# Performance work log

Hardware: AMD Instinct MI355X
Metric: run time of the kernel (lower is better)

Reference implementation:

```python
import jax, jax.numpy as jnp
import numpy as np

SEQ_LEN = 32
B, H, E, HID = 2048, 512, 512, 16
BN_EPS = 1e-5

def _mlp(x, w1, b1, g, bt, m, v, w2, b2):
    # Linear -> BatchNorm1d(eval) -> ReLU -> Linear
    h = x @ w1 + b1
    h = (h - m) * jax.lax.rsqrt(v + BN_EPS) * g + bt
    h = jnp.maximum(h, 0.0)
    return h @ w2 + b2

def setup_inputs() -> dict:
    key = jax.random.key(0)
    ks = jax.random.split(key, 24)
    def rn(k, shp, s=0.05):
        return jax.random.normal(k, shp, dtype=jnp.float32) * s
    inp = {
        'last_pos': jax.random.uniform(ks[0], (B, 2), dtype=jnp.float32),
        'hh': rn(ks[1], (1, B, H), 1.0),
        'ch': rn(ks[2], (1, B, H), 1.0),
        'se_w1': rn(ks[3], (2, HID)),
        'se_b1': rn(ks[4], (HID,)),
        'se_g': jax.random.uniform(ks[5], (HID,), dtype=jnp.float32) + 0.5,
        'se_bt': rn(ks[6], (HID,)),
        'se_m': rn(ks[7], (HID,)),
        'se_v': jax.random.uniform(ks[8], (HID,), dtype=jnp.float32) + 0.5,
        'se_w2': rn(ks[9], (HID, E)),
        'se_b2': rn(ks[10], (E,)),
        'w_ih': rn(ks[11], (4 * H, E)),
        'w_hh': rn(ks[12], (4 * H, H)),
        'b_ih': rn(ks[13], (4 * H,)),
        'b_hh': rn(ks[14], (4 * H,)),
        'hp_w1': rn(ks[15], (H, HID)),
        'hp_b1': rn(ks[16], (HID,)),
        'hp_g': jax.random.uniform(ks[17], (HID,), dtype=jnp.float32) + 0.5,
        'hp_bt': rn(ks[18], (HID,)),
        'hp_m': rn(ks[19], (HID,)),
        'hp_v': jax.random.uniform(ks[20], (HID,), dtype=jnp.float32) + 0.5,
        'hp_w2': rn(ks[21], (HID, 2)),
        'hp_b2': rn(ks[22], (2,)),
    }
    return inp

def reference(last_pos, hh, ch, se_w1, se_b1, se_g, se_bt, se_m, se_v, se_w2, se_b2,
              w_ih, w_hh, b_ih, b_hh,
              hp_w1, hp_b1, hp_g, hp_bt, hp_m, hp_v, hp_w2, hp_b2):
    h0, c0 = hh[0], ch[0]  # num_layers == 1

    def step(carry, _):
        h, c, lp = carry
        x = _mlp(lp, se_w1, se_b1, se_g, se_bt, se_m, se_v, se_w2, se_b2)  # [B,E]
        gates = x @ w_ih.T + b_ih + h @ w_hh.T + b_hh                      # [B,4H]
        i, f, g, o = jnp.split(gates, 4, axis=-1)
        i = jax.nn.sigmoid(i)
        f = jax.nn.sigmoid(f)
        g = jnp.tanh(g)
        o = jax.nn.sigmoid(o)
        c = f * c + i * g
        h = o * jnp.tanh(c)
        pos_rel = _mlp(h, hp_w1, hp_b1, hp_g, hp_bt, hp_m, hp_v, hp_w2, hp_b2)  # [B,2]
        # relative_to_abs on a length-1 sequence == pos_rel + last_pos, then sigmoid
        lp = jax.nn.sigmoid(pos_rel + lp)
        return (h, c, lp), lp

    _, traj = jax.lax.scan(step, (h0, c0, last_pos), None, length=SEQ_LEN)
    return traj  # [seq_len, batch, 2]
```

## Files before the change

### kernel.cpp

```cpp
#include <hip/hip_runtime.h>


#define TSEQ  32
#define BATCH 2048
#define HDIM  512
#define NBLK  256
#define NTHR  512
#define DEPTH 8

typedef __bf16 bf16x8 __attribute__((ext_vector_type(8)));
typedef float  f32x16 __attribute__((ext_vector_type(16)));
typedef unsigned u32x4 __attribute__((ext_vector_type(4)));
typedef unsigned long long u64;

#define BS_OFF     0
#define HPW_OFF    131072
#define UNI_OFF    147456
#define H1_OFF     157696
#define LPS_OFF    161792
#define PRM_OFF    162816
#define LDS_TOTAL  163360
#define W1T_OFF    32768
#define BT_OFF     41472

#define WS_FLAGS  0
#define WS_HATOM  2048

__device__ __forceinline__ unsigned f2bf(float f) {
  unsigned u = __float_as_uint(f);
  u += 0x7fffu + ((u >> 16) & 1u);
  return u >> 16;
}
__device__ __forceinline__ void st8(void* p, u64 v) {
  __hip_atomic_store((u64*)p, v, __ATOMIC_RELAXED, __HIP_MEMORY_SCOPE_AGENT);
}
__device__ __forceinline__ unsigned ld4(const unsigned* p) {
  return __hip_atomic_load(p, __ATOMIC_RELAXED, __HIP_MEMORY_SCOPE_AGENT);
}
__device__ __forceinline__ void st4(unsigned* p, unsigned v) {
  __hip_atomic_store(p, v, __ATOMIC_RELAXED, __HIP_MEMORY_SCOPE_AGENT);
}
__device__ __forceinline__ u32x4 ld16_dev(const void* p) {
  u32x4 r;
  asm volatile("global_load_dwordx4 %0, %1, off sc0 sc1"
               : "=&v"(r) : "v"(p) : "memory");
  return r;
}
__device__ __forceinline__ void vm_drain() {
  asm volatile("s_waitcnt vmcnt(0)" ::: "memory");
}
#define WAITV(n) do { asm volatile("s_waitcnt vmcnt(" #n ")" ::: "memory"); \
                      __builtin_amdgcn_sched_barrier(0); } while (0)

#define QB(x, imm) __uint_as_float((unsigned)__builtin_amdgcn_mov_dpp((int)__float_as_uint(x), imm, 0xF, 0xF, true))

struct KParams {
  const float *last_pos, *hh, *ch0, *w_hh, *w_ih, *b_ih, *b_hh;
  const float *se_w1, *se_b1, *se_g, *se_bt, *se_m, *se_v, *se_w2, *se_b2;
  const float *hp_w1, *hp_b1, *hp_g, *hp_bt, *hp_m, *hp_v, *hp_w2, *hp_b2;
  char* hatom;
  unsigned* flags;
  float* out;
};

__global__ __launch_bounds__(NTHR, 2) void decoder_persist(KParams p) {
  extern __shared__ char lds[];
  const int tid  = threadIdx.x;
  const int lane = tid & 63;
  const int wid  = tid >> 6;
  const int wm   = wid >> 1;
  const int wn   = wid & 1;
  const int mt   = blockIdx.x >> 4;
  const int nt   = blockIdx.x & 15;
  const int m0   = mt * 128;

  float* prm = (float*)(lds + PRM_OFF);
  float* lps = (float*)(lds + LPS_OFF);
  float* h2s = (float*)(lds + UNI_OFF);
  unsigned short* hPsh = (unsigned short*)(lds + UNI_OFF);
  float* W1T = (float*)(lds + W1T_OFF);
  float* bT  = (float*)(lds + BT_OFF);

  const int n0 = wn * 64 + (lane & 31);
  const int n1 = n0 + 32;
  const int gate = lane & 3;
  const int khalf = lane >> 5;
  const int pj = ((tid >> 8) << 1) | ((tid >> 5) & 1);
  const int pm = ((tid >> 6) & 3) * 32 + (tid & 31);

  if (tid < 16) {
    int q = tid;
    float sA = p.se_g[q] * rsqrtf(p.se_v[q] + 1e-5f);
    prm[q]      = sA;
    prm[16 + q] = (p.se_b1[q] - p.se_m[q]) * sA + p.se_bt[q];
    float hA = p.hp_g[q] * rsqrtf(p.hp_v[q] + 1e-5f);
    prm[32 + q] = hA;
    prm[48 + q] = (p.hp_b1[q] - p.hp_m[q]) * hA + p.hp_bt[q];
  }
  if (tid < 32) { prm[64 + tid] = p.se_w1[tid]; prm[96 + tid] = p.hp_w2[tid]; }
  if (tid < 2)  { prm[128 + tid] = p.hp_b2[tid]; }
  if (tid < 256) lps[tid] = p.last_pos[(size_t)m0 * 2 + tid];

  for (int a = tid; a < 2048; a += NTHR) {
    int n = a >> 6, k8 = a & 63;
    uint4 v = {0, 0, 0, 0};
    if (n <= 16) {
      const float* src = (n < 16) ? (p.se_w2 + (size_t)n * 512 + k8 * 8)
                                  : (p.se_b2 + k8 * 8);
      v.x = f2bf(src[0]) | (f2bf(src[1]) << 16);
      v.y = f2bf(src[2]) | (f2bf(src[3]) << 16);
      v.z = f2bf(src[4]) | (f2bf(src[5]) << 16);
      v.w = f2bf(src[6]) | (f2bf(src[7]) << 16);
    }
    *(uint4*)(lds + BS_OFF + ((size_t)(n * 64 + (k8 ^ (n & 7)))) * 16) = v;
  }
  __syncthreads();

  if ((wid & 1) == 0) {
    int rloc = wm * 32 + (lane & 31);
    int grow = (rloc & 3) * 512 + nt * 32 + (rloc >> 2);
    const float* arow = p.w_ih + (size_t)grow * 512;
    f32x16 accW;
    #pragma unroll
    for (int i = 0; i < 16; ++i) accW[i] = 0.f;
    float4 pa[4], pb[4];
    #pragma unroll
    for (int j = 0; j < 4; ++j) {
      int kal = j * 2 + khalf;
      pa[j] = ((const float4*)(arow + kal * 8))[0];
      pb[j] = ((const float4*)(arow + kal * 8))[1];
    }
    #pragma unroll
    for (int c = 0; c < 32; ++c) {
      int kal = c * 2 + khalf;
      union { unsigned short s[8]; bf16x8 v; } av;
      float4 a = pa[c & 3], b = pb[c & 3];
      av.s[0] = f2bf(a.x); av.s[1] = f2bf(a.y); av.s[2] = f2bf(a.z); av.s[3] = f2bf(a.w);
      av.s[4] = f2bf(b.x); av.s[5] = f2bf(b.y); av.s[6] = f2bf(b.z); av.s[7] = f2bf(b.w);
      if (c + 4 < 32) {
        int kn = (c + 4) * 2 + khalf;
        pa[c & 3] = ((const float4*)(arow + kn * 8))[0];
        pb[c & 3] = ((const float4*)(arow + kn * 8))[1];
      }
      int q = lane & 31;
      bf16x8 bp = *(const bf16x8*)(lds + BS_OFF + (((q << 6) + (kal ^ (q & 7))) << 4));
      accW = __builtin_amdgcn_mfma_f32_32x32x16_bf16(av.v, bp, accW, 0, 0, 0);
    }
    int q = lane & 31;
    #pragma unroll
    for (int r = 0; r < 16; ++r) {
      int row = (r & 3) + 8 * (r >> 2) + 4 * khalf + wm * 32;
      if (q < 16) {
        W1T[row * 17 + q] = accW[r];
      } else if (q == 16) {
        int g2 = (row & 3) * 512 + nt * 32 + (row >> 2);
        bT[row] = accW[r] + p.b_ih[g2] + p.b_hh[g2];
      }
    }
  }
  __syncthreads();

  union BW { unsigned short s[8]; bf16x8 v; } w0f, w1f;
  #pragma unroll
  for (int j = 0; j < 8; ++j) {
    w0f.s[j] = (unsigned short)f2bf(W1T[n0 * 17 + khalf * 8 + j]);
    w1f.s[j] = (unsigned short)f2bf(W1T[n1 * 17 + khalf * 8 + j]);
  }
  float biasr[2];
  biasr[0] = bT[wn * 64 + (lane & 31)];
  biasr[1] = bT[wn * 64 + 32 + (lane & 31)];
  {
    const float* src = p.hh + (size_t)(m0 + pm) * 512 + nt * 32 + pj * 8;
    float4 f0 = ((const float4*)src)[0];
    float4 f1 = ((const float4*)src)[1];
    u64 lo = (u64)f2bf(f0.x) | ((u64)f2bf(f0.y) << 16)
           | ((u64)f2bf(f0.z) << 32) | ((u64)f2bf(f0.w) << 48);
    u64 hi = (u64)f2bf(f1.x) | ((u64)f2bf(f1.y) << 16)
           | ((u64)f2bf(f1.z) << 32) | ((u64)f2bf(f1.w) << 48);
    u64* hdst = (u64*)(p.hatom + 2097152 + mt * 131072);
    st8(hdst + (512 * nt + tid) * 2,     lo);
    st8(hdst + (512 * nt + tid) * 2 + 1, hi);
  }
  __syncthreads();
  if (tid == 0) st4(p.flags + mt * 32 + nt, 1u);

  for (int a = tid; a < 8192; a += NTHR) {
    int n = a >> 6, ka = a & 63;
    int grow = (n & 3) * 512 + nt * 32 + (n >> 2);
    const float* src = p.w_hh + (size_t)grow * 512 + ka * 8;
    uint4 v;
    v.x = f2bf(src[0]) | (f2bf(src[1]) << 16);
    v.y = f2bf(src[2]) | (f2bf(src[3]) << 16);
    v.z = f2bf(src[4]) | (f2bf(src[5]) << 16);
    v.w = f2bf(src[6]) | (f2bf(src[7]) << 16);
    *(uint4*)(lds + BS_OFF + ((size_t)(n * 64 + (ka ^ (n & 7)))) * 16) = v;
  }
  for (int a = tid; a < 1024; a += NTHR) {
    int n = a >> 6, k8 = a & 63;
    const float* src = p.hp_w1 + (size_t)(k8 * 8) * 16 + n;
    uint4 v;
    v.x = f2bf(src[0])  | (f2bf(src[16]) << 16);
    v.y = f2bf(src[32]) | (f2bf(src[48]) << 16);
    v.z = f2bf(src[64]) | (f2bf(src[80]) << 16);
    v.w = f2bf(src[96]) | (f2bf(src[112]) << 16);
    *(uint4*)(lds + HPW_OFF + ((size_t)(n * 64 + (k8 ^ (n & 7)))) * 16) = v;
  }
  float c_st[2][16];
  #pragma unroll
  for (int t2 = 0; t2 < 2; ++t2)
    #pragma unroll
    for (int r = 0; r < 16; ++r) c_st[t2][r] = 0.f;
  if ((lane & 3) == 0) {
    #pragma unroll
    for (int t2 = 0; t2 < 2; ++t2) {
      int jj = (wn * 64 + t2 * 32 + (lane & 31)) >> 2;
      #pragma unroll
      for (int r = 0; r < 16; ++r) {
        int row = (r & 3) + 8 * (r >> 2) + 4 * khalf + wm * 32;
        c_st[t2][r] = p.ch0[(size_t)(m0 + row) * 512 + nt * 32 + jj];
      }
    }
  }
  __syncthreads();

  float sA2q = 0.f, bA2q = 0.f;
  if ((lane & 31) < 16) { sA2q = prm[32 + (lane & 31)]; bA2q = prm[48 + (lane & 31)]; }
  const unsigned* fl = p.flags + mt * 32 + (lane & 15);

  for (int t = 0; t < TSEQ; ++t) {
    if (wid == 0) {
      while (!__all((int)(ld4(fl) >= (unsigned)(t + 1))))
        __builtin_amdgcn_s_sleep(2);
    }
    __syncthreads();

    f32x16 acc0, acc1, accP;
    #pragma unroll
    for (int i = 0; i < 16; ++i) { acc0[i] = 0.f; acc1[i] = 0.f; accP[i] = 0.f; }
    {
      const char* abase = p.hatom + (size_t)((t + 1) & 1) * 2097152 + mt * 131072
                          + (wm * 64 + lane) * 16;
      vm_drain();
      u32x4 pre[DEPTH];
      #pragma unroll
      for (int c = 0; c < DEPTH; ++c) pre[c] = ld16_dev(abase + c * 4096);
      union AB { u32x4 u; bf16x8 v; };
      #pragma unroll
      for (int c = 0; c < 32; ++c) {
        switch (c) {
          default: WAITV(7); break;
          case 25: WAITV(6); break;
          case 26: WAITV(5); break;
          case 27: WAITV(4); break;
          case 28: WAITV(3); break;
          case 29: WAITV(2); break;
          case 30: WAITV(1); break;
          case 31: WAITV(0); break;
        }
        AB u;
        u.u = pre[c & (DEPTH - 1)];
        if (c + DEPTH < 32)
          pre[c & (DEPTH - 1)] = ld16_dev(abase + (c + DEPTH) * 4096);
        int kal = c * 2 + khalf;
        bf16x8 b0 = *(const bf16x8*)(lds + BS_OFF + (((n0 << 6) + (kal ^ (n0 & 7))) << 4));
        bf16x8 b1 = *(const bf16x8*)(lds + BS_OFF + (((n1 << 6) + (kal ^ (n1 & 7))) << 4));
        acc0 = __builtin_amdgcn_mfma_f32_32x32x16_bf16(u.v, b0, acc0, 0, 0, 0);
        acc1 = __builtin_amdgcn_mfma_f32_32x32x16_bf16(u.v, b1, acc1, 0, 0, 0);
        if (wn == 0) {
          bf16x8 bp = {};
          if ((lane & 31) < 16)
            bp = *(const bf16x8*)(lds + HPW_OFF
                  + ((((lane & 31) << 6) + (kal ^ (lane & 7))) << 4));
          accP = __builtin_amdgcn_mfma_f32_32x32x16_bf16(u.v, bp, accP, 0, 0, 0);
        }
      }
    }

    if (t > 0) {
      if (wn == 0 && (lane & 31) < 16) {
        int q = lane & 31;
        #pragma unroll
        for (int r = 0; r < 16; ++r) {
          int row = (r & 3) + 8 * (r >> 2) + 4 * khalf + wm * 32;
          h2s[row * 20 + q] = fmaxf(accP[r] * sA2q + bA2q, 0.f);
        }
      }
      __syncthreads();
    }

    if (tid < 256) {
      int m = tid >> 1, c = tid & 1;
      float lp0, lp1;
      if (t > 0) {
        float a2 = prm[128 + c];
        const float4* hrow = (const float4*)(lds + UNI_OFF + m * 80);
        #pragma unroll
        for (int g4 = 0; g4 < 4; ++g4) {
          float4 v = hrow[g4];
          a2 += v.x * prm[96 + (g4 * 4 + 0) * 2 + c];
          a2 += v.y * prm[96 + (g4 * 4 + 1) * 2 + c];
          a2 += v.z * prm[96 + (g4 * 4 + 2) * 2 + c];
          a2 += v.w * prm[96 + (g4 * 4 + 3) * 2 + c];
        }
        float lpv = 1.f / (1.f + __expf(-(a2 + lps[tid])));
        lps[tid] = lpv;
        if (nt == 0)
          p.out[((size_t)(t - 1) * BATCH + m0 + m) * 2 + c] = lpv;
        float other = QB(lpv, 0xB1);
        lp0 = c ? other : lpv;
        lp1 = c ? lpv : other;
      } else {
        lp0 = lps[m * 2];
        lp1 = lps[m * 2 + 1];
      }
      u64 hq[2];
      #pragma unroll
      for (int half = 0; half < 2; ++half) {
        u64 w = 0;
        #pragma unroll
        for (int i = 0; i < 4; ++i) {
          int q = c * 8 + half * 4 + i;
          float z = lp0 * prm[64 + q] + lp1 * prm[80 + q];
          w |= (u64)f2bf(fmaxf(z * prm[q] + prm[16 + q], 0.f)) << (16 * i);
        }
        hq[half] = w;
      }
      u64* hd = (u64*)(lds + H1_OFF + m * 32 + c * 16);
      hd[0] = hq[0];
      hd[1] = hq[1];
    }
    __syncthreads();

    {
      bf16x8 a1 = *(const bf16x8*)(lds + H1_OFF + (wm * 32 + (lane & 31)) * 32 + khalf * 16);
      acc0 = __builtin_amdgcn_mfma_f32_32x32x16_bf16(a1, w0f.v, acc0, 0, 0, 0);
      acc1 = __builtin_amdgcn_mfma_f32_32x32x16_bf16(a1, w1f.v, acc1, 0, 0, 0);
    }

    #pragma unroll
    for (int t2 = 0; t2 < 2; ++t2) {
      float bias = biasr[t2];
      int jj = (wn * 64 + t2 * 32 + (lane & 31)) >> 2;
      float act[16];
      const f32x16& A = (t2 == 0) ? acc0 : acc1;
      #pragma unroll
      for (int r = 0; r < 16; ++r) {
        float v = A[r] + bias;
        float vv = (gate == 2) ? 2.f * v : v;
        float sg = 1.f / (1.f + __expf(-vv));
        act[r] = (gate == 2) ? 2.f * sg - 1.f : sg;
      }
      #pragma unroll
      for (int r = 0; r < 16; ++r) {
        float iv = QB(act[r], 0x00);
        float fv = QB(act[r], 0x55);
        float gv = QB(act[r], 0xAA);
        float ov = QB(act[r], 0xFF);
        float cn = fv * c_st[t2][r] + iv * gv;
        c_st[t2][r] = cn;
        float th = 2.f / (1.f + __expf(-2.f * cn)) - 1.f;
        float hn = ov * th;
        if ((lane & 3) == 0) {
          int row = (r & 3) + 8 * (r >> 2) + 4 * khalf + wm * 32;
          hPsh[row * 36 + jj] = (unsigned short)f2bf(hn);
        }
      }
    }
    __syncthreads();

    {
      const u64* hp8 = (const u64*)(lds + UNI_OFF + pm * 72 + pj * 16);
      u64* hdst = (u64*)(p.hatom + (size_t)(t & 1) * 2097152 + mt * 131072);
      st8(hdst + (512 * nt + tid) * 2,     hp8[0]);
      st8(hdst + (512 * nt + tid) * 2 + 1, hp8[1]);
    }
    __syncthreads();
    if (tid == 0) st4(p.flags + mt * 32 + nt, (unsigned)(t + 2));
  }

  {
    if (wid == 0) {
      while (!__all((int)(ld4(fl) >= (unsigned)(TSEQ + 1))))
        __builtin_amdgcn_s_sleep(2);
    }
    __syncthreads();
    f32x16 accP;
    #pragma unroll
    for (int i = 0; i < 16; ++i) accP[i] = 0.f;
    if (wn == 0) {
      const char* abase = p.hatom + 2097152 + mt * 131072 + (wm * 64 + lane) * 16;
      vm_drain();
      u32x4 pre[DEPTH];
      #pragma unroll
      for (int c = 0; c < DEPTH; ++c) pre[c] = ld16_dev(abase + c * 4096);
      union AB { u32x4 u; bf16x8 v; };
      #pragma unroll
      for (int c = 0; c < 32; ++c) {
        switch (c) {
          default: WAITV(7); break;
          case 25: WAITV(6); break;
          case 26: WAITV(5); break;
          case 27: WAITV(4); break;
          case 28: WAITV(3); break;
          case 29: WAITV(2); break;
          case 30: WAITV(1); break;
          case 31: WAITV(0); break;
        }
        AB u;
        u.u = pre[c & (DEPTH - 1)];
        if (c + DEPTH < 32)
          pre[c & (DEPTH - 1)] = ld16_dev(abase + (c + DEPTH) * 4096);
        int kal = c * 2 + khalf;
        bf16x8 bp = {};
        if ((lane & 31) < 16)
          bp = *(const bf16x8*)(lds + HPW_OFF
                + ((((lane & 31) << 6) + (kal ^ (lane & 7))) << 4));
        accP = __builtin_amdgcn_mfma_f32_32x32x16_bf16(u.v, bp, accP, 0, 0, 0);
      }
      if ((lane & 31) < 16) {
        int q = lane & 31;
        #pragma unroll
        for (int r = 0; r < 16; ++r) {
          int row = (r & 3) + 8 * (r >> 2) + 4 * khalf + wm * 32;
          h2s[row * 20 + q] = fmaxf(accP[r] * sA2q + bA2q, 0.f);
        }
      }
    }
    __syncthreads();
    if (tid < 256 && nt == 0) {
      int m = tid >> 1, c = tid & 1;
      float a2 = prm[128 + c];
      const float4* hrow = (const float4*)(lds + UNI_OFF + m * 80);
      #pragma unroll
      for (int g4 = 0; g4 < 4; ++g4) {
        float4 v = hrow[g4];
        a2 += v.x * prm[96 + (g4 * 4 + 0) * 2 + c];
        a2 += v.y * prm[96 + (g4 * 4 + 1) * 2 + c];
        a2 += v.z * prm[96 + (g4 * 4 + 2) * 2 + c];
        a2 += v.w * prm[96 + (g4 * 4 + 3) * 2 + c];
      }
      float lpv = 1.f / (1.f + __expf(-(a2 + lps[tid])));
      p.out[((size_t)(TSEQ - 1) * BATCH + m0 + m) * 2 + c] = lpv;
    }
  }
}

extern "C" void kernel_launch(void* const* d_in, const int* in_sizes, int n_in,
                              void* d_out, int out_size, void* d_ws, size_t ws_size,
                              hipStream_t stream) {
  char* ws = (char*)d_ws;
  KParams kp;
  kp.last_pos = (const float*)d_in[0];
  kp.hh    = (const float*)d_in[1];
  kp.ch0   = (const float*)d_in[2];
  kp.se_w1 = (const float*)d_in[3];
  kp.se_b1 = (const float*)d_in[4];
  kp.se_g  = (const float*)d_in[5];
  kp.se_bt = (const float*)d_in[6];
  kp.se_m  = (const float*)d_in[7];
  kp.se_v  = (const float*)d_in[8];
  kp.se_w2 = (const float*)d_in[9];
  kp.se_b2 = (const float*)d_in[10];
  kp.w_ih  = (const float*)d_in[11];
  kp.w_hh  = (const float*)d_in[12];
  kp.b_ih  = (const float*)d_in[13];
  kp.b_hh  = (const float*)d_in[14];
  kp.hp_w1 = (const float*)d_in[15];
  kp.hp_b1 = (const float*)d_in[16];
  kp.hp_g  = (const float*)d_in[17];
  kp.hp_bt = (const float*)d_in[18];
  kp.hp_m  = (const float*)d_in[19];
  kp.hp_v  = (const float*)d_in[20];
  kp.hp_w2 = (const float*)d_in[21];
  kp.hp_b2 = (const float*)d_in[22];
  kp.flags = (unsigned*)(ws + WS_FLAGS);
  kp.hatom = ws + WS_HATOM;
  kp.out   = (float*)d_out;

  (void)hipMemsetAsync(ws + WS_FLAGS, 0, 2048, stream);
  (void)hipFuncSetAttribute((const void*)decoder_persist,
                            hipFuncAttributeMaxDynamicSharedMemorySize, LDS_TOTAL);
  decoder_persist<<<dim3(NBLK), dim3(NTHR), LDS_TOTAL, stream>>>(kp);
}
```

Measured before the change: 537.9 us.

## Remap persistent blocks by XCC so row groups share L2 and use sc0 traffic

At startup each block reads its XCC id, publishes it to a workspace table and waits until every block has done so. Blocks are then renumbered so the 16 blocks sharing a row tile (mt) sit on the same XCC where possible. For row tiles that fall entirely within one XCC, the h exchange loads and stores use sc0-only (XCC-coherent, L2-cached) accesses instead of device-scope sc0 sc1, which aims to cut cross-die latency on each timestep's dependency. This adds a global startup barrier and relies on the hardware XCC assignment and the coherence semantics of sc0 being correct.

After: 542.5 us. About the same (+0.9%).

```diff
diff --git a/kernel.cpp b/kernel.cpp
--- a/kernel.cpp
+++ b/kernel.cpp
@@ -24,7 +24,8 @@
 #define BT_OFF     41472
 
 #define WS_FLAGS  0
-#define WS_HATOM  2048
+#define WS_XCC    2048
+#define WS_HATOM  4096
 
 __device__ __forceinline__ unsigned f2bf(float f) {
   unsigned u = __float_as_uint(f);
@@ -46,6 +47,16 @@
                : "=&v"(r) : "v"(p) : "memory");
   return r;
 }
+__device__ __forceinline__ u32x4 ld16_sc0(const void* p) {
+  u32x4 r;
+  asm volatile("global_load_dwordx4 %0, %1, off sc0"
+               : "=&v"(r) : "v"(p) : "memory");
+  return r;
+}
+__device__ __forceinline__ void st16_sc0(void* p, u32x4 v) {
+  asm volatile("global_store_dwordx4 %0, %1, off sc0"
+               :: "v"(p), "v"(v) : "memory");
+}
 __device__ __forceinline__ void vm_drain() {
   asm volatile("s_waitcnt vmcnt(0)" ::: "memory");
 }
@@ -53,6 +64,72 @@
                       __builtin_amdgcn_sched_barrier(0); } while (0)
 
 #define QB(x, imm) __uint_as_float((unsigned)__builtin_amdgcn_mov_dpp((int)__float_as_uint(x), imm, 0xF, 0xF, true))
+
+#define GEMM_BODY(LDFN)                                                          \
+  {                                                                              \
+    vm_drain();                                                                  \
+    u32x4 pre[DEPTH];                                                            \
+    _Pragma("unroll")                                                            \
+    for (int c = 0; c < DEPTH; ++c) pre[c] = LDFN(abase + c * 4096);             \
+    _Pragma("unroll")                                                            \
+    for (int c = 0; c < 32; ++c) {                                               \
+      switch (c) {                                                               \
+        default: WAITV(7); break;                                                \
+        case 25: WAITV(6); break;                                                \
+        case 26: WAITV(5); break;                                                \
+        case 27: WAITV(4); break;                                                \
+        case 28: WAITV(3); break;                                                \
+        case 29: WAITV(2); break;                                                \
+        case 30: WAITV(1); break;                                                \
+        case 31: WAITV(0); break;                                                \
+      }                                                                          \
+      union ABu { u32x4 u; bf16x8 v; } u;                                        \
+      u.u = pre[c & (DEPTH - 1)];                                                \
+      if (c + DEPTH < 32) pre[c & (DEPTH - 1)] = LDFN(abase + (c + DEPTH) * 4096); \
+      int kal = c * 2 + khalf;                                                   \
+      bf16x8 b0 = *(const bf16x8*)(lds + BS_OFF + (((n0 << 6) + (kal ^ (n0 & 7))) << 4)); \
+      bf16x8 b1 = *(const bf16x8*)(lds + BS_OFF + (((n1 << 6) + (kal ^ (n1 & 7))) << 4)); \
+      acc0 = __builtin_amdgcn_mfma_f32_32x32x16_bf16(u.v, b0, acc0, 0, 0, 0);    \
+      acc1 = __builtin_amdgcn_mfma_f32_32x32x16_bf16(u.v, b1, acc1, 0, 0, 0);    \
+      if (wn == 0) {                                                             \
+        bf16x8 bp = {};                                                          \
+        if ((lane & 31) < 16)                                                    \
+          bp = *(const bf16x8*)(lds + HPW_OFF                                    \
+                + ((((lane & 31) << 6) + (kal ^ (lane & 7))) << 4));             \
+        accP = __builtin_amdgcn_mfma_f32_32x32x16_bf16(u.v, bp, accP, 0, 0, 0);  \
+      }                                                                          \
+    }                                                                            \
+  }
+
+#define GEMM_TAIL(LDFN)                                                          \
+  {                                                                              \
+    vm_drain();                                                                  \
+    u32x4 pre[DEPTH];                                                            \
+    _Pragma("unroll")                                                            \
+    for (int c = 0; c < DEPTH; ++c) pre[c] = LDFN(abase + c * 4096);             \
+    _Pragma("unroll")                                                            \
+    for (int c = 0; c < 32; ++c) {                                               \
+      switch (c) {                                                               \
+        default: WAITV(7); break;                                                \
+        case 25: WAITV(6); break;                                                \
+        case 26: WAITV(5); break;                                                \
+        case 27: WAITV(4); break;                                                \
+        case 28: WAITV(3); break;                                                \
+        case 29: WAITV(2); break;                                                \
+        case 30: WAITV(1); break;                                                \
+        case 31: WAITV(0); break;                                                \
+      }                                                                          \
+      union ABt { u32x4 u; bf16x8 v; } u;                                        \
+      u.u = pre[c & (DEPTH - 1)];                                                \
+      if (c + DEPTH < 32) pre[c & (DEPTH - 1)] = LDFN(abase + (c + DEPTH) * 4096); \
+      int kal = c * 2 + khalf;                                                   \
+      bf16x8 bp = {};                                                            \
+      if ((lane & 31) < 16)                                                      \
+        bp = *(const bf16x8*)(lds + HPW_OFF                                      \
+              + ((((lane & 31) << 6) + (kal ^ (lane & 7))) << 4));               \
+      accP = __builtin_amdgcn_mfma_f32_32x32x16_bf16(u.v, bp, accP, 0, 0, 0);    \
+    }                                                                            \
+  }
 
 struct KParams {
   const float *last_pos, *hh, *ch0, *w_hh, *w_ih, *b_ih, *b_hh;
@@ -60,6 +137,7 @@
   const float *hp_w1, *hp_b1, *hp_g, *hp_bt, *hp_m, *hp_v, *hp_w2, *hp_b2;
   char* hatom;
   unsigned* flags;
+  unsigned* xcc;
   float* out;
 };
 
@@ -70,9 +148,36 @@
   const int wid  = tid >> 6;
   const int wm   = wid >> 1;
   const int wn   = wid & 1;
-  const int mt   = blockIdx.x >> 4;
-  const int nt   = blockIdx.x & 15;
-  const int m0   = mt * 128;
+  const int bid  = blockIdx.x;
+
+  int xcc;
+  asm volatile("s_getreg_b32 %0, hwreg(HW_REG_XCC_ID)" : "=s"(xcc));
+  xcc &= 7;
+  if (tid == 0) st4(p.xcc + bid, (unsigned)xcc + 1u);
+  unsigned* xtab = (unsigned*)(lds + BS_OFF);
+  if (tid < NBLK) {
+    unsigned v = ld4(p.xcc + tid);
+    while (v == 0) { __builtin_amdgcn_s_sleep(8); v = ld4(p.xcc + tid); }
+    xtab[tid] = v - 1u;
+  }
+  __syncthreads();
+  int rank = 0, pfx = 0, cntx = 0;
+  {
+    unsigned me = (unsigned)xcc;
+    for (int b = 0; b < NBLK; ++b) {
+      unsigned v = xtab[b];
+      rank += (b < bid && v == me) ? 1 : 0;
+      pfx  += (v < me) ? 1 : 0;
+      cntx += (v == me) ? 1 : 0;
+    }
+  }
+  const int g  = pfx + rank;
+  const int mt = __builtin_amdgcn_readfirstlane(g >> 4);
+  const int nt = __builtin_amdgcn_readfirstlane(g & 15);
+  const bool pure = (bool)__builtin_amdgcn_readfirstlane(
+      (int)(pfx <= mt * 16 && mt * 16 + 16 <= pfx + cntx));
+  const int m0 = mt * 128;
+  __syncthreads();
 
   float* prm = (float*)(lds + PRM_OFF);
   float* lps = (float*)(lds + LPS_OFF);
@@ -173,13 +278,23 @@
     const float* src = p.hh + (size_t)(m0 + pm) * 512 + nt * 32 + pj * 8;
     float4 f0 = ((const float4*)src)[0];
     float4 f1 = ((const float4*)src)[1];
-    u64 lo = (u64)f2bf(f0.x) | ((u64)f2bf(f0.y) << 16)
-           | ((u64)f2bf(f0.z) << 32) | ((u64)f2bf(f0.w) << 48);
-    u64 hi = (u64)f2bf(f1.x) | ((u64)f2bf(f1.y) << 16)
-           | ((u64)f2bf(f1.z) << 32) | ((u64)f2bf(f1.w) << 48);
-    u64* hdst = (u64*)(p.hatom + 2097152 + mt * 131072);
-    st8(hdst + (512 * nt + tid) * 2,     lo);
-    st8(hdst + (512 * nt + tid) * 2 + 1, hi);
+    char* hd = p.hatom + 2097152 + mt * 131072 + (size_t)(512 * nt + tid) * 16;
+    if (pure) {
+      u32x4 hv;
+      hv.x = f2bf(f0.x) | (f2bf(f0.y) << 16);
+      hv.y = f2bf(f0.z) | (f2bf(f0.w) << 16);
+      hv.z = f2bf(f1.x) | (f2bf(f1.y) << 16);
+      hv.w = f2bf(f1.z) | (f2bf(f1.w) << 16);
+      st16_sc0(hd, hv);
+    } else {
+      u64 lo = (u64)f2bf(f0.x) | ((u64)f2bf(f0.y) << 16)
+             | ((u64)f2bf(f0.z) << 32) | ((u64)f2bf(f0.w) << 48);
+      u64 hi = (u64)f2bf(f1.x) | ((u64)f2bf(f1.y) << 16)
+             | ((u64)f2bf(f1.z) << 32) | ((u64)f2bf(f1.w) << 48);
+      st8(hd, lo);
+      st8(hd + 8, hi);
+    }
+    vm_drain();
   }
   __syncthreads();
   if (tid == 0) st4(p.flags + mt * 32 + nt, 1u);
@@ -240,40 +355,8 @@
     {
       const char* abase = p.hatom + (size_t)((t + 1) & 1) * 2097152 + mt * 131072
                           + (wm * 64 + lane) * 16;
-      vm_drain();
-      u32x4 pre[DEPTH];
-      #pragma unroll
-      for (int c = 0; c < DEPTH; ++c) pre[c] = ld16_dev(abase + c * 4096);
-      union AB { u32x4 u; bf16x8 v; };
-      #pragma unroll
-      for (int c = 0; c < 32; ++c) {
-        switch (c) {
-          default: WAITV(7); break;
-          case 25: WAITV(6); break;
-          case 26: WAITV(5); break;
-          case 27: WAITV(4); break;
-          case 28: WAITV(3); break;
-          case 29: WAITV(2); break;
-          case 30: WAITV(1); break;
-          case 31: WAITV(0); break;
-        }
-        AB u;
-        u.u = pre[c & (DEPTH - 1)];
-        if (c + DEPTH < 32)
-          pre[c & (DEPTH - 1)] = ld16_dev(abase + (c + DEPTH) * 4096);
-        int kal = c * 2 + khalf;
-        bf16x8 b0 = *(const bf16x8*)(lds + BS_OFF + (((n0 << 6) + (kal ^ (n0 & 7))) << 4));
-        bf16x8 b1 = *(const bf16x8*)(lds + BS_OFF + (((n1 << 6) + (kal ^ (n1 & 7))) << 4));
-        acc0 = __builtin_amdgcn_mfma_f32_32x32x16_bf16(u.v, b0, acc0, 0, 0, 0);
-        acc1 = __builtin_amdgcn_mfma_f32_32x32x16_bf16(u.v, b1, acc1, 0, 0, 0);
-        if (wn == 0) {
-          bf16x8 bp = {};
-          if ((lane & 31) < 16)
-            bp = *(const bf16x8*)(lds + HPW_OFF
-                  + ((((lane & 31) << 6) + (kal ^ (lane & 7))) << 4));
-          accP = __builtin_amdgcn_mfma_f32_32x32x16_bf16(u.v, bp, accP, 0, 0, 0);
-        }
-      }
+      if (pure) GEMM_BODY(ld16_sc0)
+      else      GEMM_BODY(ld16_dev)
     }
 
     if (t > 0) {
@@ -370,9 +453,19 @@
 
     {
       const u64* hp8 = (const u64*)(lds + UNI_OFF + pm * 72 + pj * 16);
-      u64* hdst = (u64*)(p.hatom + (size_t)(t & 1) * 2097152 + mt * 131072);
-      st8(hdst + (512 * nt + tid) * 2,     hp8[0]);
-      st8(hdst + (512 * nt + tid) * 2 + 1, hp8[1]);
+      u64 a = hp8[0], b = hp8[1];
+      char* hd = p.hatom + (size_t)(t & 1) * 2097152 + mt * 131072
+               + (size_t)(512 * nt + tid) * 16;
+      if (pure) {
+        u32x4 hv;
+        hv.x = (unsigned)a; hv.y = (unsigned)(a >> 32);
+        hv.z = (unsigned)b; hv.w = (unsigned)(b >> 32);
+        st16_sc0(hd, hv);
+      } else {
+        st8(hd, a);
+        st8(hd + 8, b);
+      }
+      vm_drain();
     }
     __syncthreads();
     if (tid == 0) st4(p.flags + mt * 32 + nt, (unsigned)(t + 2));
@@ -389,34 +482,8 @@
     for (int i = 0; i < 16; ++i) accP[i] = 0.f;
     if (wn == 0) {
       const char* abase = p.hatom + 2097152 + mt * 131072 + (wm * 64 + lane) * 16;
-      vm_drain();
-      u32x4 pre[DEPTH];
-      #pragma unroll
-      for (int c = 0; c < DEPTH; ++c) pre[c] = ld16_dev(abase + c * 4096);
-      union AB { u32x4 u; bf16x8 v; };
-      #pragma unroll
-      for (int c = 0; c < 32; ++c) {
-        switch (c) {
-          default: WAITV(7); break;
-          case 25: WAITV(6); break;
-          case 26: WAITV(5); break;
-          case 27: WAITV(4); break;
-          case 28: WAITV(3); break;
-          case 29: WAITV(2); break;
-          case 30: WAITV(1); break;
-          case 31: WAITV(0); break;
-        }
-        AB u;
-        u.u = pre[c & (DEPTH - 1)];
-        if (c + DEPTH < 32)
-          pre[c & (DEPTH - 1)] = ld16_dev(abase + (c + DEPTH) * 4096);
-        int kal = c * 2 + khalf;
-        bf16x8 bp = {};
-        if ((lane & 31) < 16)
-          bp = *(const bf16x8*)(lds + HPW_OFF
-                + ((((lane & 31) << 6) + (kal ^ (lane & 7))) << 4));
-        accP = __builtin_amdgcn_mfma_f32_32x32x16_bf16(u.v, bp, accP, 0, 0, 0);
-      }
+      if (pure) GEMM_TAIL(ld16_sc0)
+      else      GEMM_TAIL(ld16_dev)
       if ((lane & 31) < 16) {
         int q = lane & 31;
         #pragma unroll
@@ -474,10 +541,11 @@
   kp.hp_w2 = (const float*)d_in[21];
   kp.hp_b2 = (const float*)d_in[22];
   kp.flags = (unsigned*)(ws + WS_FLAGS);
+  kp.xcc   = (unsigned*)(ws + WS_XCC);
   kp.hatom = ws + WS_HATOM;
   kp.out   = (float*)d_out;
 
-  (void)hipMemsetAsync(ws + WS_FLAGS, 0, 2048, stream);
+  (void)hipMemsetAsync(ws + WS_FLAGS, 0, 3072, stream);
   (void)hipFuncSetAttribute((const void*)decoder_persist,
                             hipFuncAttributeMaxDynamicSharedMemorySize, LDS_TOTAL);
   decoder_persist<<<dim3(NBLK), dim3(NTHR), LDS_TOTAL, stream>>>(kp);
```

## Replace whole-row flag barrier with progressive per-chunk prefix gating

Applied to the files above, without the earlier changes.

The block no longer waits for all 16 producer blocks of its row tile before reading the shared hidden state. Wave 0 polls the flags and publishes the contiguous prefix of finished producers as a token in LDS. Every wave then gates each K-chunk load only on the producers that chunk (plus its prefetch depth) depends on, so MFMA work can start while later producers are still finishing. In exchange there is more polling inside the hot loop, wave 0's flag load drains the vector-memory counter, and the block-wide __syncthreads is removed.

Result: slower. 578.3 us (+7.5%).

```diff
diff --git a/kernel.cpp b/kernel.cpp
--- a/kernel.cpp
+++ b/kernel.cpp
@@ -19,7 +19,8 @@
 #define H1_OFF     157696
 #define LPS_OFF    161792
 #define PRM_OFF    162816
-#define LDS_TOTAL  163360
+#define TOK_OFF    163360
+#define LDS_TOTAL  163368
 #define W1T_OFF    32768
 #define BT_OFF     41472
 
@@ -33,9 +34,6 @@
 }
 __device__ __forceinline__ void st8(void* p, u64 v) {
   __hip_atomic_store((u64*)p, v, __ATOMIC_RELAXED, __HIP_MEMORY_SCOPE_AGENT);
-}
-__device__ __forceinline__ unsigned ld4(const unsigned* p) {
-  return __hip_atomic_load(p, __ATOMIC_RELAXED, __HIP_MEMORY_SCOPE_AGENT);
 }
 __device__ __forceinline__ void st4(unsigned* p, unsigned v) {
   __hip_atomic_store(p, v, __ATOMIC_RELAXED, __HIP_MEMORY_SCOPE_AGENT);
@@ -46,6 +44,12 @@
                : "=&v"(r) : "v"(p) : "memory");
   return r;
 }
+__device__ __forceinline__ unsigned ld4_drain(const unsigned* p) {
+  unsigned r;
+  asm volatile("global_load_dword %0, %1, off sc0 sc1\n\ts_waitcnt vmcnt(0)"
+               : "=v"(r) : "v"(p) : "memory");
+  return r;
+}
 __device__ __forceinline__ void vm_drain() {
   asm volatile("s_waitcnt vmcnt(0)" ::: "memory");
 }
@@ -53,6 +57,28 @@
                       __builtin_amdgcn_sched_barrier(0); } while (0)
 
 #define QB(x, imm) __uint_as_float((unsigned)__builtin_amdgcn_mov_dpp((int)__float_as_uint(x), imm, 0xF, 0xF, true))
+
+#define GATE(REQ, TT)                                                          \
+  do {                                                                         \
+    if (wid == 0) {                                                            \
+      while (pfx < (REQ)) {                                                    \
+        unsigned fv = ld4_drain(flp);                                          \
+        unsigned m16 = (unsigned)__ballot((int)(fv >= (unsigned)((TT) + 1)))   \
+                       & 0xFFFFu;                                              \
+        pfx = (int)__builtin_ctz(~m16 | 0x10000u);                             \
+        if (lane == 0) *tok = (TT) * 16 + pfx;                                 \
+        if (pfx < (REQ)) __builtin_amdgcn_s_sleep(1);                          \
+      }                                                                        \
+    } else {                                                                   \
+      if (tokr < (TT) * 16 + (REQ)) {                                          \
+        while ((tokr = *tok) < (TT) * 16 + (REQ))                              \
+          __builtin_amdgcn_s_sleep(1);                                         \
+      }                                                                        \
+    }                                                                          \
+    __builtin_amdgcn_sched_barrier(0);                                         \
+  } while (0)
+
+#define REQC(c) ((((c) + DEPTH) >> 1) + 1 > 16 ? 16 : (((c) + DEPTH) >> 1) + 1)
 
 struct KParams {
   const float *last_pos, *hh, *ch0, *w_hh, *w_ih, *b_ih, *b_hh;
@@ -80,6 +106,7 @@
   unsigned short* hPsh = (unsigned short*)(lds + UNI_OFF);
   float* W1T = (float*)(lds + W1T_OFF);
   float* bT  = (float*)(lds + BT_OFF);
+  volatile int* tok = (volatile int*)(lds + TOK_OFF);
 
   const int n0 = wn * 64 + (lane & 31);
   const int n1 = n0 + 32;
@@ -100,6 +127,7 @@
   if (tid < 32) { prm[64 + tid] = p.se_w1[tid]; prm[96 + tid] = p.hp_w2[tid]; }
   if (tid < 2)  { prm[128 + tid] = p.hp_b2[tid]; }
   if (tid < 256) lps[tid] = p.last_pos[(size_t)m0 * 2 + tid];
+  if (tid == 0) *tok = 0;
 
   for (int a = tid; a < 2048; a += NTHR) {
     int n = a >> 6, k8 = a & 63;
@@ -225,21 +253,18 @@
 
   float sA2q = 0.f, bA2q = 0.f;
   if ((lane & 31) < 16) { sA2q = prm[32 + (lane & 31)]; bA2q = prm[48 + (lane & 31)]; }
-  const unsigned* fl = p.flags + mt * 32 + (lane & 15);
+  const unsigned* flp = p.flags + mt * 32 + (lane & 15);
+  int tokr = 0;
 
   for (int t = 0; t < TSEQ; ++t) {
-    if (wid == 0) {
-      while (!__all((int)(ld4(fl) >= (unsigned)(t + 1))))
-        __builtin_amdgcn_s_sleep(2);
-    }
-    __syncthreads();
-
     f32x16 acc0, acc1, accP;
     #pragma unroll
     for (int i = 0; i < 16; ++i) { acc0[i] = 0.f; acc1[i] = 0.f; accP[i] = 0.f; }
     {
       const char* abase = p.hatom + (size_t)((t + 1) & 1) * 2097152 + mt * 131072
                           + (wm * 64 + lane) * 16;
+      int pfx = 0;
+      GATE(4, t);
       vm_drain();
       u32x4 pre[DEPTH];
       #pragma unroll
@@ -247,6 +272,7 @@
       union AB { u32x4 u; bf16x8 v; };
       #pragma unroll
       for (int c = 0; c < 32; ++c) {
+        GATE(REQC(c), t);
         switch (c) {
           default: WAITV(7); break;
           case 25: WAITV(6); break;
@@ -379,16 +405,13 @@
   }
 
   {
-    if (wid == 0) {
-      while (!__all((int)(ld4(fl) >= (unsigned)(TSEQ + 1))))
-        __builtin_amdgcn_s_sleep(2);
-    }
-    __syncthreads();
     f32x16 accP;
     #pragma unroll
     for (int i = 0; i < 16; ++i) accP[i] = 0.f;
     if (wn == 0) {
       const char* abase = p.hatom + 2097152 + mt * 131072 + (wm * 64 + lane) * 16;
+      int pfx = 0;
+      GATE(4, TSEQ);
       vm_drain();
       u32x4 pre[DEPTH];
       #pragma unroll
@@ -396,6 +419,7 @@
       union AB { u32x4 u; bf16x8 v; };
       #pragma unroll
       for (int c = 0; c < 32; ++c) {
+        GATE(REQC(c), TSEQ);
         switch (c) {
           default: WAITV(7); break;
           case 25: WAITV(6); break;
```
